# Performance work log

Measured on AMD Instinct MI355X. Metric: run time of the kernel, lower is better.

The kernel has to match this reference:

```python
import jax, jax.numpy as jnp
import numpy as np

N = 8192      # number of points
K = 64        # max_num_neighbors in radius()
C_IN = 64     # input feature channels
R = 0.125     # radius r


def setup_inputs() -> dict:
    key = jax.random.key(0)
    ks = jax.random.split(key, 8)
    s = 0.05
    return {
        "x": jax.random.normal(ks[0], (N, C_IN), jnp.float32),
        "pos": jax.random.uniform(ks[1], (N, 3), jnp.float32),
        "batch": jnp.zeros((N,), jnp.int32),
        "W1": jax.random.normal(ks[2], (C_IN + 3, 64), jnp.float32) * s,
        "b1": jnp.zeros((64,), jnp.float32),
        "W2": jax.random.normal(ks[3], (64, 128), jnp.float32) * s,
        "b2": jnp.zeros((128,), jnp.float32),
        "Wg": jax.random.normal(ks[4], (128, 256), jnp.float32) * s,
        "bg": jnp.zeros((256,), jnp.float32),
    }


def reference(x, pos, batch, W1, b1, W2, b2, Wg, bg):
    # --- radius neighbor search (K nearest within radius R, self included) ---
    sq = jnp.sum(pos * pos, axis=-1)                     # [N]
    d2 = sq[:, None] + sq[None, :] - 2.0 * (pos @ pos.T)  # [N, N] squared dists
    same = batch[:, None] == batch[None, :]
    d2 = jnp.where(same, d2, jnp.inf)
    neg_d2, idx = jax.lax.top_k(-d2, K)                  # [N, K] nearest K per target
    valid = (-neg_d2) <= R * R                           # within-radius mask; self always valid

    # --- PointConv message: feature_nn(concat(x_j, pos_j - pos_i)) ---
    rel = pos[idx] - pos[:, None, :]                     # [N, K, 3]
    feat = jnp.concatenate([x[idx], rel], axis=-1)       # [N, K, C_IN+3]
    h = jax.nn.relu(feat @ W1 + b1)                      # [N, K, 64]
    h = jax.nn.relu(h @ W2 + b2)                         # [N, K, 128]

    # --- max aggregation over neighbors ---
    h = jnp.where(valid[..., None], h, -jnp.inf)
    agg = jnp.max(h, axis=1)                             # [N, 128]

    # --- global_nn ---
    out = jax.nn.relu(agg @ Wg + bg)                     # [N, 256]
    return out
```

## Files before the change

### kernel.cpp

```cpp
#include <hip/hip_runtime.h>

#define N_PTS 8192
#define R2F 0.015625f

__global__ __launch_bounds__(256) void k_g(const float* __restrict__ x,
                                           const float* __restrict__ W1,
                                           float* __restrict__ g) {
    __shared__ float xs[32][68];
    __shared__ float ws_[64][64];
    const int t = threadIdx.x;
    const int r0 = blockIdx.x * 32;
    for (int v = t; v < 1024; v += 256)
        ((float4*)&ws_[0][0])[v] = ((const float4*)W1)[v];
    for (int v = t; v < 512; v += 256) {
        const int n = v >> 4, c4 = (v & 15) * 4;
        *(float4*)&xs[n][c4] = *(const float4*)&x[(r0 + n) * 64 + c4];
    }
    __syncthreads();
    const int c0 = (t & 15) * 4, n0 = (t >> 4) * 2;
    float acc[2][4];
    #pragma unroll
    for (int ni = 0; ni < 2; ++ni)
        #pragma unroll
        for (int ci = 0; ci < 4; ++ci) acc[ni][ci] = 0.0f;
    #pragma unroll
    for (int kb4 = 0; kb4 < 16; ++kb4) {
        float4 av[2], wv[4];
        #pragma unroll
        for (int ni = 0; ni < 2; ++ni)
            av[ni] = *(const float4*)&xs[n0 + ni][kb4 * 4];
        #pragma unroll
        for (int ki = 0; ki < 4; ++ki)
            wv[ki] = *(const float4*)&ws_[kb4 * 4 + ki][c0];
        #pragma unroll
        for (int ki = 0; ki < 4; ++ki) {
            #pragma unroll
            for (int ni = 0; ni < 2; ++ni) {
                const float a = (&av[ni].x)[ki];
                acc[ni][0] = __fmaf_rn(a, wv[ki].x, acc[ni][0]);
                acc[ni][1] = __fmaf_rn(a, wv[ki].y, acc[ni][1]);
                acc[ni][2] = __fmaf_rn(a, wv[ki].z, acc[ni][2]);
                acc[ni][3] = __fmaf_rn(a, wv[ki].w, acc[ni][3]);
            }
        }
    }
    #pragma unroll
    for (int ni = 0; ni < 2; ++ni)
        *(float4*)&g[(r0 + n0 + ni) * 64 + c0] =
            make_float4(acc[ni][0], acc[ni][1], acc[ni][2], acc[ni][3]);
}

union U0 {
    struct { unsigned mb[4][64]; unsigned mj[4][64]; } s;
    float gs[64][68];
};

__global__ __launch_bounds__(256) void fused_all(const float* __restrict__ g,
                                                 const float* __restrict__ pos,
                                                 const float* __restrict__ W1,
                                                 const float* __restrict__ b1,
                                                 const float* __restrict__ W2,
                                                 const float* __restrict__ b2,
                                                 const float* __restrict__ Wg,
                                                 const float* __restrict__ bg,
                                                 float* __restrict__ out) {
    __shared__ U0    u0;
    __shared__ float pmw[4][128];
    __shared__ float aggS[128];
    __shared__ unsigned selb[64];
    __shared__ int   selj[64];
    __shared__ int   nvalidS;

    const int t    = threadIdx.x;
    const int lane = t & 63;
    const int w    = t >> 6;
    const int qb   = w << 11;
    const int i    = blockIdx.x;

    const float xi = pos[i * 3 + 0], yi = pos[i * 3 + 1], zi = pos[i * 3 + 2];
    const float sqi = __fadd_rn(__fadd_rn(__fmul_rn(xi, xi), __fmul_rn(yi, yi)),
                                __fmul_rn(zi, zi));

    unsigned kb[32];
    unsigned m1b = 0xFFFFFFFFu, m2b = 0xFFFFFFFFu;
    int      m1j = 0x7FFFFFFF,  m2j = 0x7FFFFFFF;
    #pragma unroll
    for (int k = 0; k < 32; ++k) {
        const int j = qb + lane + (k << 6);
        const float xj = pos[j * 3 + 0], yj = pos[j * 3 + 1], zj = pos[j * 3 + 2];
        const float sqj = __fadd_rn(__fadd_rn(__fmul_rn(xj, xj), __fmul_rn(yj, yj)),
                                    __fmul_rn(zj, zj));
        const float dot = __fmaf_rn(zi, zj, __fmaf_rn(yi, yj, __fmul_rn(xi, xj)));
        const float d2  = __fsub_rn(__fadd_rn(sqi, sqj), __fmul_rn(2.0f, dot));
        unsigned b = __float_as_uint(d2);
        b = (b & 0x80000000u) ? ~b : (b | 0x80000000u);
        kb[k] = b;
        if (b < m1b)      { m2b = m1b; m2j = m1j; m1b = b; m1j = j; }
        else if (b < m2b) { m2b = b;   m2j = j; }
    }

    u0.s.mb[w][lane] = 0xFFFFFFFFu;
    u0.s.mj[w][lane] = 0xFFFFFF00u | (unsigned)((w << 6) | lane);

    unsigned removed = 0u;
    int      level = 0;
    unsigned lb = m1b;
    int      lj = m1j;
    for (int s = 0; s < 64; ++s) {
        unsigned rb = lb;
        int      rj = lj;
        #pragma unroll
        for (int off = 32; off > 0; off >>= 1) {
            const unsigned ob = (unsigned)__shfl_down((int)rb, off);
            const int      oj = __shfl_down(rj, off);
            if (ob < rb || (ob == rb && oj < rj)) { rb = ob; rj = oj; }
        }
        const unsigned wb = (unsigned)__shfl((int)rb, 0);
        const int      wj = __shfl(rj, 0);
        const unsigned db = (wb & 0x80000000u) ? (wb ^ 0x80000000u) : ~wb;
        if (!(__uint_as_float(db) <= R2F)) break;
        if (lane == 0) { u0.s.mb[w][s] = wb; u0.s.mj[w][s] = (unsigned)wj; }
        if (lb == wb && lj == wj) {
            removed |= 1u << ((wj - qb - lane) >> 6);
            ++level;
            if (level == 1) { lb = m2b; lj = m2j; }
            else {
                lb = 0xFFFFFFFFu; lj = 0x7FFFFFFF;
                #pragma unroll
                for (int k = 0; k < 32; ++k) {
                    if (!(removed & (1u << k))) {
                        const unsigned b = kb[k];
                        if (b < lb) { lb = b; lj = qb + lane + (k << 6); }
                    }
                }
            }
        }
    }
    __syncthreads();

    {
        const int p = lane;
        const unsigned be = u0.s.mb[w][p];
        const unsigned je = u0.s.mj[w][p];
        int rank = p;
        #pragma unroll
        for (int d = 1; d < 4; ++d) {
            const int wp = (w + d) & 3;
            int lo = 0;
            #pragma unroll
            for (int st = 32; st > 0; st >>= 1) {
                const int idx = lo + st - 1;
                const unsigned ob = u0.s.mb[wp][idx];
                const unsigned oj = u0.s.mj[wp][idx];
                if (ob < be || (ob == be && oj < je)) lo += st;
            }
            {
                const unsigned ob = u0.s.mb[wp][lo];
                const unsigned oj = u0.s.mj[wp][lo];
                if (ob < be || (ob == be && oj < je)) lo += 1;
            }
            rank += lo;
        }
        if (rank < 64) { selb[rank] = be; selj[rank] = (int)(je & 8191u); }
    }
    __syncthreads();

    for (int v = t; v < 1024; v += 256) {
        const int n = v >> 4, c4 = (v & 15) * 4;
        *(float4*)&u0.gs[n][c4] = *(const float4*)&g[selj[n] * 64 + c4];
    }
    {
        bool ok = false;
        if (t < 64) {
            const unsigned b = selb[t];
            const unsigned db = (b & 0x80000000u) ? (b ^ 0x80000000u) : ~b;
            ok = (__uint_as_float(db) <= R2F);
        }
        const unsigned long long vm = __ballot(ok);
        if (t == 0) nvalidS = __popcll(vm);
    }
    __syncthreads();
    const int nvalid = nvalidS;

    {
        const int c0 = (t & 15) * 4, n0 = (t >> 4) * 4;
        float rr[4][3];
        #pragma unroll
        for (int ni = 0; ni < 4; ++ni) {
            const int j = selj[n0 + ni];
            rr[ni][0] = pos[j * 3 + 0] - xi;
            rr[ni][1] = pos[j * 3 + 1] - yi;
            rr[ni][2] = pos[j * 3 + 2] - zi;
        }
        float w1b[3][4], bb[4];
        #pragma unroll
        for (int ci = 0; ci < 4; ++ci) {
            w1b[0][ci] = W1[4096 + c0 + ci];
            w1b[1][ci] = W1[4160 + c0 + ci];
            w1b[2][ci] = W1[4224 + c0 + ci];
            bb[ci]     = b1[c0 + ci];
        }
        #pragma unroll
        for (int ni = 0; ni < 4; ++ni) {
            const int n = n0 + ni;
            const float4 gv = *(const float4*)&u0.gs[n][c0];
            float4 hv;
            #pragma unroll
            for (int ci = 0; ci < 4; ++ci) {
                float a = (&gv.x)[ci];
                a = __fmaf_rn(rr[ni][0], w1b[0][ci], a);
                a = __fmaf_rn(rr[ni][1], w1b[1][ci], a);
                a = __fmaf_rn(rr[ni][2], w1b[2][ci], a);
                a = fmaxf(a + bb[ci], 0.0f);
                (&hv.x)[ci] = (n < nvalid) ? a : 0.0f;
            }
            *(float4*)&u0.gs[n][c0] = hv;
        }
    }
    __syncthreads();

    {
        const float (*h1)[68] = u0.gs;
        const int c4 = (t & 15) * 4;
        const int nb = (t >> 4) * 4;
        float acc[4][8];
        #pragma unroll
        for (int ni = 0; ni < 4; ++ni)
            #pragma unroll
            for (int k = 0; k < 8; ++k) acc[ni][k] = 0.0f;

        #pragma unroll 4
        for (int ccb = 0; ccb < 16; ++ccb) {
            float4 av[4];
            #pragma unroll
            for (int ni = 0; ni < 4; ++ni)
                av[ni] = *(const float4*)&h1[nb + ni][ccb * 4];
            #pragma unroll
            for (int ci = 0; ci < 4; ++ci) {
                const int cc = ccb * 4 + ci;
                const float4 w0 = *(const float4*)&W2[cc * 128 + c4];
                const float4 w1 = *(const float4*)&W2[cc * 128 + c4 + 64];
                const float wv[8] = {w0.x, w0.y, w0.z, w0.w, w1.x, w1.y, w1.z, w1.w};
                #pragma unroll
                for (int k = 0; k < 8; ++k) {
                    acc[0][k] = __fmaf_rn((&av[0].x)[ci], wv[k], acc[0][k]);
                    acc[1][k] = __fmaf_rn((&av[1].x)[ci], wv[k], acc[1][k]);
                    acc[2][k] = __fmaf_rn((&av[2].x)[ci], wv[k], acc[2][k]);
                    acc[3][k] = __fmaf_rn((&av[3].x)[ci], wv[k], acc[3][k]);
                }
            }
        }
        float m8[8];
        #pragma unroll
        for (int k = 0; k < 8; ++k) {
            const int ch = (k < 4) ? (c4 + k) : (64 + c4 + k - 4);
            const float bb = b2[ch];
            float mm = 0.0f;
            #pragma unroll
            for (int ni = 0; ni < 4; ++ni)
                if (nb + ni < nvalid) mm = fmaxf(mm, acc[ni][k] + bb);
            m8[k] = mm;
        }
        #pragma unroll
        for (int k = 0; k < 8; ++k) {
            float v = m8[k];
            v = fmaxf(v, __shfl_down(v, 32));
            v = fmaxf(v, __shfl_down(v, 16));
            m8[k] = v;
        }
        if ((t & 63) < 16) {
            #pragma unroll
            for (int k = 0; k < 4; ++k) pmw[w][c4 + k]          = m8[k];
            #pragma unroll
            for (int k = 4; k < 8; ++k) pmw[w][64 + c4 + k - 4] = m8[k];
        }
    }
    __syncthreads();

    if (t < 128)
        aggS[t] = fmaxf(fmaxf(pmw[0][t], pmw[1][t]),
                        fmaxf(pmw[2][t], pmw[3][t]));
    __syncthreads();

    {
        float acc = 0.0f;
        #pragma unroll 8
        for (int k = 0; k < 128; ++k)
            acc = __fmaf_rn(aggS[k], Wg[k * 256 + t], acc);
        out[i * 256 + t] = fmaxf(acc + bg[t], 0.0f);
    }
}

extern "C" void kernel_launch(void* const* d_in, const int* in_sizes, int n_in,
                              void* d_out, int out_size, void* d_ws, size_t ws_size,
                              hipStream_t stream) {
    const float* x   = (const float*)d_in[0];
    const float* pos = (const float*)d_in[1];
    const float* W1 = (const float*)d_in[3];
    const float* b1 = (const float*)d_in[4];
    const float* W2 = (const float*)d_in[5];
    const float* b2 = (const float*)d_in[6];
    const float* Wg = (const float*)d_in[7];
    const float* bg = (const float*)d_in[8];
    float* out = (float*)d_out;

    float* g = (float*)d_ws;

    k_g<<<N_PTS / 32, 256, 0, stream>>>(x, W1, g);
    fused_all<<<N_PTS, 256, 0, stream>>>(g, pos, W1, b1, W2, b2, Wg, bg, out);
}
```

Measured before the change: 421.3 us.

## Cut register pressure in fused kernel to raise occupancy via recompute

```diff
diff --git a/kernel.cpp b/kernel.cpp
--- a/kernel.cpp
+++ b/kernel.cpp
@@ -50,20 +50,32 @@
             make_float4(acc[ni][0], acc[ni][1], acc[ni][2], acc[ni][3]);
 }
 
+__device__ __forceinline__ unsigned d2key(const float* __restrict__ pos, int j,
+                                          float xi, float yi, float zi,
+                                          float sqi) {
+    const float xj = pos[j * 3 + 0], yj = pos[j * 3 + 1], zj = pos[j * 3 + 2];
+    const float sqj = __fadd_rn(__fadd_rn(__fmul_rn(xj, xj), __fmul_rn(yj, yj)),
+                                __fmul_rn(zj, zj));
+    const float dot = __fmaf_rn(zi, zj, __fmaf_rn(yi, yj, __fmul_rn(xi, xj)));
+    const float d2  = __fsub_rn(__fadd_rn(sqi, sqj), __fmul_rn(2.0f, dot));
+    unsigned b = __float_as_uint(d2);
+    return (b & 0x80000000u) ? ~b : (b | 0x80000000u);
+}
+
 union U0 {
     struct { unsigned mb[4][64]; unsigned mj[4][64]; } s;
     float gs[64][68];
 };
 
-__global__ __launch_bounds__(256) void fused_all(const float* __restrict__ g,
-                                                 const float* __restrict__ pos,
-                                                 const float* __restrict__ W1,
-                                                 const float* __restrict__ b1,
-                                                 const float* __restrict__ W2,
-                                                 const float* __restrict__ b2,
-                                                 const float* __restrict__ Wg,
-                                                 const float* __restrict__ bg,
-                                                 float* __restrict__ out) {
+__global__ __launch_bounds__(256, 10) void fused_all(const float* __restrict__ g,
+                                                     const float* __restrict__ pos,
+                                                     const float* __restrict__ W1,
+                                                     const float* __restrict__ b1,
+                                                     const float* __restrict__ W2,
+                                                     const float* __restrict__ b2,
+                                                     const float* __restrict__ Wg,
+                                                     const float* __restrict__ bg,
+                                                     float* __restrict__ out) {
     __shared__ U0    u0;
     __shared__ float pmw[4][128];
     __shared__ float aggS[128];
@@ -81,22 +93,25 @@
     const float sqi = __fadd_rn(__fadd_rn(__fmul_rn(xi, xi), __fmul_rn(yi, yi)),
                                 __fmul_rn(zi, zi));
 
-    unsigned kb[32];
-    unsigned m1b = 0xFFFFFFFFu, m2b = 0xFFFFFFFFu;
-    int      m1j = 0x7FFFFFFF,  m2j = 0x7FFFFFFF;
+    unsigned m1b = 0xFFFFFFFFu, m2b = 0xFFFFFFFFu,
+             m3b = 0xFFFFFFFFu, m4b = 0xFFFFFFFFu;
+    int      m1j = 0x7FFFFFFF,  m2j = 0x7FFFFFFF,
+             m3j = 0x7FFFFFFF,  m4j = 0x7FFFFFFF;
     #pragma unroll
     for (int k = 0; k < 32; ++k) {
         const int j = qb + lane + (k << 6);
-        const float xj = pos[j * 3 + 0], yj = pos[j * 3 + 1], zj = pos[j * 3 + 2];
-        const float sqj = __fadd_rn(__fadd_rn(__fmul_rn(xj, xj), __fmul_rn(yj, yj)),
-                                    __fmul_rn(zj, zj));
-        const float dot = __fmaf_rn(zi, zj, __fmaf_rn(yi, yj, __fmul_rn(xi, xj)));
-        const float d2  = __fsub_rn(__fadd_rn(sqi, sqj), __fmul_rn(2.0f, dot));
-        unsigned b = __float_as_uint(d2);
-        b = (b & 0x80000000u) ? ~b : (b | 0x80000000u);
-        kb[k] = b;
-        if (b < m1b)      { m2b = m1b; m2j = m1j; m1b = b; m1j = j; }
-        else if (b < m2b) { m2b = b;   m2j = j; }
+        const unsigned b = d2key(pos, j, xi, yi, zi, sqi);
+        if (b < m1b) {
+            m4b = m3b; m4j = m3j; m3b = m2b; m3j = m2j;
+            m2b = m1b; m2j = m1j; m1b = b;   m1j = j;
+        } else if (b < m2b) {
+            m4b = m3b; m4j = m3j; m3b = m2b; m3j = m2j;
+            m2b = b;   m2j = j;
+        } else if (b < m3b) {
+            m4b = m3b; m4j = m3j; m3b = b;   m3j = j;
+        } else if (b < m4b) {
+            m4b = b;   m4j = j;
+        }
     }
 
     u0.s.mb[w][lane] = 0xFFFFFFFFu;
@@ -123,14 +138,17 @@
         if (lb == wb && lj == wj) {
             removed |= 1u << ((wj - qb - lane) >> 6);
             ++level;
-            if (level == 1) { lb = m2b; lj = m2j; }
+            if      (level == 1) { lb = m2b; lj = m2j; }
+            else if (level == 2) { lb = m3b; lj = m3j; }
+            else if (level == 3) { lb = m4b; lj = m4j; }
             else {
                 lb = 0xFFFFFFFFu; lj = 0x7FFFFFFF;
-                #pragma unroll
+                #pragma unroll 4
                 for (int k = 0; k < 32; ++k) {
                     if (!(removed & (1u << k))) {
-                        const unsigned b = kb[k];
-                        if (b < lb) { lb = b; lj = qb + lane + (k << 6); }
+                        const int jr = qb + lane + (k << 6);
+                        const unsigned b = d2key(pos, jr, xi, yi, zi, sqi);
+                        if (b < lb) { lb = b; lj = jr; }
                     }
                 }
             }
@@ -223,56 +241,55 @@
         const float (*h1)[68] = u0.gs;
         const int c4 = (t & 15) * 4;
         const int nb = (t >> 4) * 4;
-        float acc[4][8];
-        #pragma unroll
-        for (int ni = 0; ni < 4; ++ni)
-            #pragma unroll
-            for (int k = 0; k < 8; ++k) acc[ni][k] = 0.0f;
-
-        #pragma unroll 4
-        for (int ccb = 0; ccb < 16; ++ccb) {
-            float4 av[4];
+        #pragma unroll
+        for (int half = 0; half < 2; ++half) {
+            const int ch0 = half * 64 + c4;
+            float acc[4][4];
             #pragma unroll
             for (int ni = 0; ni < 4; ++ni)
-                av[ni] = *(const float4*)&h1[nb + ni][ccb * 4];
-            #pragma unroll
-            for (int ci = 0; ci < 4; ++ci) {
-                const int cc = ccb * 4 + ci;
-                const float4 w0 = *(const float4*)&W2[cc * 128 + c4];
-                const float4 w1 = *(const float4*)&W2[cc * 128 + c4 + 64];
-                const float wv[8] = {w0.x, w0.y, w0.z, w0.w, w1.x, w1.y, w1.z, w1.w};
-                #pragma unroll
-                for (int k = 0; k < 8; ++k) {
-                    acc[0][k] = __fmaf_rn((&av[0].x)[ci], wv[k], acc[0][k]);
-                    acc[1][k] = __fmaf_rn((&av[1].x)[ci], wv[k], acc[1][k]);
-                    acc[2][k] = __fmaf_rn((&av[2].x)[ci], wv[k], acc[2][k]);
-                    acc[3][k] = __fmaf_rn((&av[3].x)[ci], wv[k], acc[3][k]);
+                #pragma unroll
+                for (int k = 0; k < 4; ++k) acc[ni][k] = 0.0f;
+
+            #pragma unroll 4
+            for (int ccb = 0; ccb < 16; ++ccb) {
+                float4 wt[4];
+                #pragma unroll
+                for (int ci = 0; ci < 4; ++ci)
+                    wt[ci] = *(const float4*)&W2[(ccb * 4 + ci) * 128 + ch0];
+                #pragma unroll
+                for (int ni = 0; ni < 4; ++ni) {
+                    const float4 av = *(const float4*)&h1[nb + ni][ccb * 4];
+                    #pragma unroll
+                    for (int ci = 0; ci < 4; ++ci) {
+                        const float a = (&av.x)[ci];
+                        acc[ni][0] = __fmaf_rn(a, wt[ci].x, acc[ni][0]);
+                        acc[ni][1] = __fmaf_rn(a, wt[ci].y, acc[ni][1]);
+                        acc[ni][2] = __fmaf_rn(a, wt[ci].z, acc[ni][2]);
+                        acc[ni][3] = __fmaf_rn(a, wt[ci].w, acc[ni][3]);
+                    }
                 }
             }
-        }
-        float m8[8];
-        #pragma unroll
-        for (int k = 0; k < 8; ++k) {
-            const int ch = (k < 4) ? (c4 + k) : (64 + c4 + k - 4);
-            const float bb = b2[ch];
-            float mm = 0.0f;
-            #pragma unroll
-            for (int ni = 0; ni < 4; ++ni)
-                if (nb + ni < nvalid) mm = fmaxf(mm, acc[ni][k] + bb);
-            m8[k] = mm;
-        }
-        #pragma unroll
-        for (int k = 0; k < 8; ++k) {
-            float v = m8[k];
-            v = fmaxf(v, __shfl_down(v, 32));
-            v = fmaxf(v, __shfl_down(v, 16));
-            m8[k] = v;
-        }
-        if ((t & 63) < 16) {
-            #pragma unroll
-            for (int k = 0; k < 4; ++k) pmw[w][c4 + k]          = m8[k];
-            #pragma unroll
-            for (int k = 4; k < 8; ++k) pmw[w][64 + c4 + k - 4] = m8[k];
+            float m4v[4];
+            #pragma unroll
+            for (int k = 0; k < 4; ++k) {
+                const float bb = b2[ch0 + k];
+                float mm = 0.0f;
+                #pragma unroll
+                for (int ni = 0; ni < 4; ++ni)
+                    if (nb + ni < nvalid) mm = fmaxf(mm, acc[ni][k] + bb);
+                m4v[k] = mm;
+            }
+            #pragma unroll
+            for (int k = 0; k < 4; ++k) {
+                float v = m4v[k];
+                v = fmaxf(v, __shfl_down(v, 32));
+                v = fmaxf(v, __shfl_down(v, 16));
+                m4v[k] = v;
+            }
+            if ((t & 63) < 16) {
+                #pragma unroll
+                for (int k = 0; k < 4; ++k) pmw[w][ch0 + k] = m4v[k];
+            }
         }
     }
     __syncthreads();
```

After: 424.6 us. No clear change (+0.8%).
